# Kernel tuning notes

Hardware: AMD Instinct MI355X
Metric: run time of the kernel (lower is better)

Reference implementation:

```python
import jax, jax.numpy as jnp
import numpy as np

NUM_HEADS = 16


def setup_inputs() -> dict:
    key = jax.random.key(0)
    ks = jax.random.split(key, 4)
    B, S, H = 2, 2048, 1024
    hidden_states = jax.random.normal(ks[0], (B, S, H), dtype=jnp.float32)
    attention_mask = jnp.zeros((B, 1, 1, S), dtype=jnp.float32)
    scale = 1.0 / np.sqrt(H)
    Wq = jax.random.normal(ks[1], (H, H), dtype=jnp.float32) * scale
    Wk = jax.random.normal(ks[2], (H, H), dtype=jnp.float32) * scale
    Wv = jax.random.normal(ks[3], (H, H), dtype=jnp.float32) * scale
    bq = jnp.zeros((H,), dtype=jnp.float32)
    bk = jnp.zeros((H,), dtype=jnp.float32)
    bv = jnp.zeros((H,), dtype=jnp.float32)
    return {"hidden_states": hidden_states, "attention_mask": attention_mask,
            "Wq": Wq, "bq": bq, "Wk": Wk, "bk": bk, "Wv": Wv, "bv": bv}


def _split_heads(x, B, S):
    # [B, S, H] -> [B, h, S, d]
    return x.reshape(B, S, NUM_HEADS, -1).transpose(0, 2, 1, 3)


def reference(hidden_states, attention_mask, Wq, bq, Wk, bk, Wv, bv):
    B, S, H = hidden_states.shape
    d = H // NUM_HEADS
    q = _split_heads(hidden_states @ Wq + bq, B, S)  # [B,h,S,d]
    k = _split_heads(hidden_states @ Wk + bk, B, S)
    v = _split_heads(hidden_states @ Wv + bv, B, S)

    scores = jnp.einsum('bhqd,bhkd->bhqk', q, k) / jnp.sqrt(jnp.float32(d))
    # causal mask: -inf strictly above diagonal, plus additive pad mask
    i = jnp.arange(S)[:, None]
    j = jnp.arange(S)[None, :]
    causal = jnp.where(j > i, -jnp.inf, 0.0).astype(scores.dtype)  # [S,S]
    scores = scores + attention_mask + causal[None, None, :, :]

    probs = jax.nn.softmax(scores, axis=-1)  # dropout prob = 0.0 -> identity
    context = jnp.einsum('bhqk,bhkd->bhqd', probs, v)  # [B,h,S,d]
    return context.transpose(0, 2, 1, 3).reshape(B, S, H)
```

## Files before the change

### kernel.cpp

```cpp
#include <hip/hip_runtime.h>

typedef __attribute__((ext_vector_type(4)))  float f32x4;
typedef __attribute__((ext_vector_type(16))) float f32x16;
typedef __attribute__((ext_vector_type(8)))  short bf16x8;

typedef __attribute__((address_space(1))) const void gvoid;
typedef __attribute__((address_space(3))) void lvoid;

__device__ __forceinline__ void gl_lds16(const void* g, void* l) {
  __builtin_amdgcn_global_load_lds((gvoid*)g, (lvoid*)l, 16, 0, 0);
}

__device__ __forceinline__ float exp2_fast(float x) {
  return __builtin_amdgcn_exp2f(x);
}

__device__ __forceinline__ ushort f2bf(float f) {
  union { float f; unsigned u; } v; v.f = f;
  unsigned u = v.u;
  return (ushort)((u + 0x7fffu + ((u >> 16) & 1u)) >> 16);
}

__device__ __forceinline__ uint cvt_pk_bf16(float lo, float hi) {
  uint r;
  asm("v_cvt_pk_bf16_f32 %0, %1, %2" : "=v"(r) : "v"(lo), "v"(hi));
  return r;
}
__device__ __forceinline__ void plswap(uint& x, uint& y) {
  asm volatile("v_permlane32_swap_b32 %0, %1" : "+v"(x), "+v"(y));
}

__global__ __launch_bounds__(256) void cvt_x(const float* __restrict__ x,
                                             ushort* __restrict__ o) {
  int idx = blockIdx.x * 256 + threadIdx.x;
  float4 v = reinterpret_cast<const float4*>(x)[idx];
  ushort4 r;
  r.x = f2bf(v.x); r.y = f2bf(v.y); r.z = f2bf(v.z); r.w = f2bf(v.w);
  reinterpret_cast<ushort4*>(o)[idx] = r;
}

__global__ __launch_bounds__(256) void wtrans(const float* __restrict__ Wq,
                                              const float* __restrict__ Wk,
                                              const float* __restrict__ Wv,
                                              ushort* __restrict__ WT) {
  __shared__ ushort tile[64 * 68];
  int bx = blockIdx.x;
  int w = bx >> 8, rem = bx & 255;
  int k0 = (rem >> 4) << 6, n0 = (rem & 15) << 6;
  const float* W = (w == 0) ? Wq : (w == 1) ? Wk : Wv;
  int tid = threadIdx.x;
#pragma unroll
  for (int it = 0; it < 4; ++it) {
    int idx = tid + it * 256;
    int r = idx >> 4, c4 = (idx & 15) * 4;
    float4 v = *reinterpret_cast<const float4*>(&W[(k0 + r) * 1024 + n0 + c4]);
    ushort4 u;
    u.x = f2bf(v.x); u.y = f2bf(v.y); u.z = f2bf(v.z); u.w = f2bf(v.w);
    *reinterpret_cast<ushort4*>(&tile[r * 68 + c4]) = u;
  }
  __syncthreads();
#pragma unroll
  for (int it = 0; it < 4; ++it) {
    int idx = tid + it * 256;
    int n = idx >> 4, k4 = (idx & 15) * 4;
    ushort4 o;
    o.x = tile[(k4 + 0) * 68 + n];
    o.y = tile[(k4 + 1) * 68 + n];
    o.z = tile[(k4 + 2) * 68 + n];
    o.w = tile[(k4 + 3) * 68 + n];
    *reinterpret_cast<ushort4*>(&WT[w * 1048576 + (size_t)(n0 + n) * 1024 + k0 + k4]) = o;
  }
}

__global__ __launch_bounds__(256) void qkv_gemm(
    const ushort* __restrict__ Xb, const ushort* __restrict__ WT,
    const float* __restrict__ bq, const float* __restrict__ bk,
    const float* __restrict__ bv, ushort* __restrict__ Qb,
    ushort* __restrict__ Kb, ushort* __restrict__ VT) {
  __shared__ ushort smem[128 * 136];
  ushort* Xs = smem;
  ushort* Ws = smem + 8192;
  int tid = threadIdx.x;
  int wave = tid >> 6, lane = tid & 63, g = lane >> 4, lr = lane & 15;
  int wr = wave >> 1, wc = wave & 1;
  int m0 = blockIdx.x << 7;
  int n0g = blockIdx.y << 7;
  f32x4 acc[4][4];
#pragma unroll
  for (int i = 0; i < 4; ++i)
#pragma unroll
    for (int j = 0; j < 4; ++j) { acc[i][j][0] = 0.f; acc[i][j][1] = 0.f; acc[i][j][2] = 0.f; acc[i][j][3] = 0.f; }

  int l3 = lane >> 3;
  int jsw = ((lane & 7) ^ l3) * 8;
  int swz = lr & 7;
  for (int k0 = 0; k0 < 1024; k0 += 64) {
    __syncthreads();
#pragma unroll
    for (int c = 0; c < 4; ++c) {
      int cw = wave * 4 + c;
      int row = cw * 8 + l3;
      gl_lds16(Xb + (size_t)(m0 + row) * 1024 + k0 + jsw, Xs + cw * 512);
      gl_lds16(WT + (size_t)(n0g + row) * 1024 + k0 + jsw, Ws + cw * 512);
    }
    __syncthreads();
#pragma unroll
    for (int ks = 0; ks < 2; ++ks) {
      bf16x8 a[4], b[4];
      int slot = ((ks * 4 + g) ^ swz) * 8;
#pragma unroll
      for (int mi = 0; mi < 4; ++mi)
        a[mi] = *reinterpret_cast<const bf16x8*>(&Xs[(wr * 64 + mi * 16 + lr) * 64 + slot]);
#pragma unroll
      for (int ni = 0; ni < 4; ++ni)
        b[ni] = *reinterpret_cast<const bf16x8*>(&Ws[(wc * 64 + ni * 16 + lr) * 64 + slot]);
#pragma unroll
      for (int mi = 0; mi < 4; ++mi)
#pragma unroll
        for (int ni = 0; ni < 4; ++ni)
          acc[mi][ni] = __builtin_amdgcn_mfma_f32_16x16x32_bf16(a[mi], b[ni], acc[mi][ni], 0, 0, 0);
    }
  }
  __syncthreads();

  int which = n0g >> 10;
  const float* bias = (which == 0) ? bq : (which == 1) ? bk : bv;
  int nloc0 = (n0g & 1023);
  if (which == 2) {
#pragma unroll
    for (int ni = 0; ni < 4; ++ni) {
      int row = wc * 64 + ni * 16 + lr;
      float bb = bias[nloc0 + row];
#pragma unroll
      for (int mi = 0; mi < 4; ++mi) {
        int m = wr * 64 + mi * 16 + g * 4;
        ushort4 v4;
        v4.x = f2bf(acc[mi][ni][0] + bb);
        v4.y = f2bf(acc[mi][ni][1] + bb);
        v4.z = f2bf(acc[mi][ni][2] + bb);
        v4.w = f2bf(acc[mi][ni][3] + bb);
        *reinterpret_cast<ushort4*>(&smem[row * 136 + m]) = v4;
      }
    }
    __syncthreads();
    int b_ = m0 >> 11, s0 = m0 & 2047;
#pragma unroll
    for (int it = 0; it < 8; ++it) {
      int c = tid + it * 256;
      int row = c >> 4, mc = (c & 15) * 8;
      uint4 vv = *reinterpret_cast<const uint4*>(&smem[row * 136 + mc]);
      int n = nloc0 + row;
      int hh = n >> 6, dd = n & 63;
      *reinterpret_cast<uint4*>(&VT[((size_t)(b_ * 16 + hh) * 64 + dd) * 2048 + s0 + mc]) = vv;
    }
  } else {
#pragma unroll
    for (int ni = 0; ni < 4; ++ni) {
      int n = wc * 64 + ni * 16 + lr;
      float bb = bias[nloc0 + n];
#pragma unroll
      for (int mi = 0; mi < 4; ++mi) {
#pragma unroll
        for (int r = 0; r < 4; ++r)
          smem[(wr * 64 + mi * 16 + g * 4 + r) * 136 + n] = f2bf(acc[mi][ni][r] + bb);
      }
    }
    __syncthreads();
    ushort* ob = (which == 0) ? Qb : Kb;
#pragma unroll
    for (int it = 0; it < 8; ++it) {
      int c = tid + it * 256;
      int row = c >> 4, nc = (c & 15) * 8;
      uint4 vv = *reinterpret_cast<const uint4*>(&smem[row * 136 + nc]);
      int m = m0 + row;
      int b_ = m >> 11, s = m & 2047;
      int n = nloc0 + nc;
      int hh = n >> 6, dd = n & 63;
      *reinterpret_cast<uint4*>(&ob[((size_t)(b_ * 16 + hh) * 2048 + s) * 64 + dd]) = vv;
    }
  }
}

__device__ __forceinline__ void softmax_state(f32x16& s, float& mrun, float& lrun,
                                              f32x16& Od0, f32x16& Od1,
                                              bf16x8& p0, bf16x8& p1) {
  float tmx = s[0];
#pragma unroll
  for (int j = 1; j < 16; ++j) tmx = fmaxf(tmx, s[j]);
  tmx = fmaxf(tmx, __shfl_xor(tmx, 32));
  if (!__all(tmx - mrun <= 11.5f)) {
    float nm = fmaxf(mrun, tmx);
    float al = exp2_fast(mrun - nm);
    mrun = nm;
    lrun *= al;
#pragma unroll
    for (int j = 0; j < 16; ++j) { Od0[j] *= al; Od1[j] *= al; }
  }
  float rs = 0.f;
#pragma unroll
  for (int j = 0; j < 16; ++j) { float p = exp2_fast(s[j] - mrun); s[j] = p; rs += p; }
  rs += __shfl_xor(rs, 32);
  lrun += rs;
  uint x0 = cvt_pk_bf16(s[0], s[1]),   y0 = cvt_pk_bf16(s[4], s[5]);
  uint x1 = cvt_pk_bf16(s[2], s[3]),   y1 = cvt_pk_bf16(s[6], s[7]);
  plswap(x0, y0); plswap(x1, y1);
  uint x2 = cvt_pk_bf16(s[8], s[9]),   y2 = cvt_pk_bf16(s[12], s[13]);
  uint x3 = cvt_pk_bf16(s[10], s[11]), y3 = cvt_pk_bf16(s[14], s[15]);
  plswap(x2, y2); plswap(x3, y3);
  union U { uint w[4]; bf16x8 v; } u0, u1;
  u0.w[0] = x0; u0.w[1] = x1; u0.w[2] = y0; u0.w[3] = y1;
  u1.w[0] = x2; u1.w[1] = x3; u1.w[2] = y2; u1.w[3] = y3;
  p0 = u0.v; p1 = u1.v;
}

__device__ __forceinline__ void attn_stage2(const ushort* Kh, const ushort* VTh,
                                            char* smem, int buf, int kv0,
                                            int ws, int l3, int jsw) {
  ushort* Ksb = (ushort*)(smem + buf * 16384);
  ushort* Vsb = Ksb + 4096;
#pragma unroll
  for (int c = 0; c < 4; ++c) {
    int ch = ws * 4 + c;
    int row = ch * 8 + l3;
    gl_lds16(Kh + (size_t)(kv0 + row) * 64 + jsw, Ksb + ch * 512);
    gl_lds16(VTh + (size_t)row * 2048 + kv0 + jsw, Vsb + ch * 512);
  }
}

__device__ __forceinline__ void attn_writeout(char* smem, int wave, int lane,
                                              const f32x16& Od0, const f32x16& Od1,
                                              float lrun, float* outp, int q0w) {
  float* Ot = (float*)smem + wave * 2176;
  int hi = lane >> 5, l31 = lane & 31;
  float rl = 1.0f / lrun;
#pragma unroll
  for (int jj = 0; jj < 4; ++jj) {
    int d0a = jj * 8 + 4 * hi;
    float4 w0, w1;
    w0.x = Od0[jj * 4 + 0] * rl; w0.y = Od0[jj * 4 + 1] * rl;
    w0.z = Od0[jj * 4 + 2] * rl; w0.w = Od0[jj * 4 + 3] * rl;
    w1.x = Od1[jj * 4 + 0] * rl; w1.y = Od1[jj * 4 + 1] * rl;
    w1.z = Od1[jj * 4 + 2] * rl; w1.w = Od1[jj * 4 + 3] * rl;
    *reinterpret_cast<float4*>(&Ot[l31 * 68 + d0a]) = w0;
    *reinterpret_cast<float4*>(&Ot[l31 * 68 + 32 + d0a]) = w1;
  }
  int qr = lane >> 1, half = lane & 1;
  const float* Orow = &Ot[qr * 68 + half * 32];
  float* og = outp + (size_t)(q0w + qr) * 1024 + half * 32;
#pragma unroll
  for (int c2 = 0; c2 < 8; ++c2)
    *reinterpret_cast<float4*>(og + c2 * 4) = *reinterpret_cast<const float4*>(Orow + c2 * 4);
}

__global__ __launch_bounds__(256) void attn(const ushort* __restrict__ Qb,
                                            const ushort* __restrict__ Kb,
                                            const ushort* __restrict__ VT,
                                            const float* __restrict__ mask,
                                            float* __restrict__ out) {
  __shared__ char smem[65536];
  const float SCALE = 0.125f * 1.44269504f;
  const float L2E = 1.44269504f;
  int tid = threadIdx.x;
  int wave = tid >> 6, lane = tid & 63;
  int strip = wave & 1, P = wave >> 1;
  int hi = lane >> 5, l31 = lane & 31;
  int l3 = lane >> 3;
  int jsw = ((lane & 7) ^ l3) * 8;
  int bid = blockIdx.x;
  int logical = (bid & 7) * 64 + (bid >> 3);
  int pi = logical & 15, bh = logical >> 4;
  int b_ = bh >> 4, h = bh & 15;
  const ushort* Qh = Qb + (size_t)bh * 131072;
  const ushort* Kh = Kb + (size_t)bh * 131072;
  const ushort* VTh = VT + (size_t)bh * 131072;
  const float* maskp = mask + b_ * 2048;
  int qa0 = pi * 64 + strip * 32;
  int qb0 = (31 - pi) * 64 + strip * 32;
  int tmax = 31 - pi;
  int nsup = (tmax + 2) >> 1;

  bf16x8 aqa[4], aqb[4];
#pragma unroll
  for (int ds = 0; ds < 4; ++ds) {
    aqa[ds] = *reinterpret_cast<const bf16x8*>(Qh + (qa0 + l31) * 64 + ds * 16 + hi * 8);
    aqb[ds] = *reinterpret_cast<const bf16x8*>(Qh + (qb0 + l31) * 64 + ds * 16 + hi * 8);
  }

  f32x16 OA0, OA1, OB0, OB1;
#pragma unroll
  for (int j = 0; j < 16; ++j) { OA0[j] = 0.f; OA1[j] = 0.f; OB0[j] = 0.f; OB1[j] = 0.f; }
  float mA = -__builtin_inff(), lA = 0.f, mB = -__builtin_inff(), lB = 0.f;

  attn_stage2(Kh, VTh, smem, P, P << 6, strip, l3, jsw);

  for (int s = 0; s < nsup; ++s) {
    __syncthreads();
    int tn = 2 * (s + 1) + P;
    if (tn <= tmax)
      attn_stage2(Kh, VTh, smem, ((s + 1) & 1) * 2 + P, tn << 6, strip, l3, jsw);
    int t = 2 * s + P;
    if (t <= tmax) {
      ushort* Ksb = (ushort*)(smem + ((s & 1) * 2 + P) * 16384);
      ushort* Vsb = Ksb + 4096;
      int kv0 = t << 6;
#pragma unroll
      for (int sub = 0; sub < 2; ++sub) {
        int kvb = kv0 + sub * 32;
        bool actA = (kvb <= qa0), actB = (kvb <= qb0);
        if (!actB && !actA) continue;
        bf16x8 kf[4];
        int krow = sub * 32 + l31;
        int ksw = krow & 7;
#pragma unroll
        for (int ds = 0; ds < 4; ++ds)
          kf[ds] = *reinterpret_cast<const bf16x8*>(Ksb + krow * 64 + (((ds * 2 + hi) ^ ksw) * 8));
        f32x16 sB, sA;
        __builtin_amdgcn_s_setprio(1);
        if (actB) {
#pragma unroll
          for (int j = 0; j < 16; ++j) sB[j] = 0.f;
#pragma unroll
          for (int ds = 0; ds < 4; ++ds)
            sB = __builtin_amdgcn_mfma_f32_32x32x16_bf16(kf[ds], aqb[ds], sB, 0, 0, 0);
        }
        if (actA) {
#pragma unroll
          for (int j = 0; j < 16; ++j) sA[j] = 0.f;
#pragma unroll
          for (int ds = 0; ds < 4; ++ds)
            sA = __builtin_amdgcn_mfma_f32_32x32x16_bf16(kf[ds], aqa[ds], sA, 0, 0, 0);
        }
        __builtin_amdgcn_s_setprio(0);

        float4 mv[4];
#pragma unroll
        for (int jj = 0; jj < 4; ++jj) {
          mv[jj] = *reinterpret_cast<const float4*>(maskp + kvb + jj * 8 + 4 * hi);
          mv[jj].x *= L2E; mv[jj].y *= L2E; mv[jj].z *= L2E; mv[jj].w *= L2E;
        }

        bf16x8 pB0, pB1, pA0, pA1;
        if (actB) {
          bool dg = (kvb == qb0);
#pragma unroll
          for (int jj = 0; jj < 4; ++jj) {
            const float* mvp = (const float*)&mv[jj];
#pragma unroll
            for (int r = 0; r < 4; ++r) {
              int j = jj * 4 + r;
              float v = sB[j] * SCALE + mvp[r];
              if (dg) {
                int kvg = kvb + jj * 8 + 4 * hi + r;
                v = (kvg > qb0 + l31) ? -__builtin_inff() : v;
              }
              sB[j] = v;
            }
          }
          softmax_state(sB, mB, lB, OB0, OB1, pB0, pB1);
        }
        if (actA) {
          bool dg = (kvb == qa0);
#pragma unroll
          for (int jj = 0; jj < 4; ++jj) {
            const float* mvp = (const float*)&mv[jj];
#pragma unroll
            for (int r = 0; r < 4; ++r) {
              int j = jj * 4 + r;
              float v = sA[j] * SCALE + mvp[r];
              if (dg) {
                int kvg = kvb + jj * 8 + 4 * hi + r;
                v = (kvg > qa0 + l31) ? -__builtin_inff() : v;
              }
              sA[j] = v;
            }
          }
          softmax_state(sA, mA, lA, OA0, OA1, pA0, pA1);
        }

        __builtin_amdgcn_s_setprio(1);
#pragma unroll
        for (int ks = 0; ks < 2; ++ks) {
#pragma unroll
          for (int h2 = 0; h2 < 2; ++h2) {
            int drow = h2 * 32 + l31;
            bf16x8 vf = *reinterpret_cast<const bf16x8*>(
                Vsb + drow * 64 + (((sub * 4 + ks * 2 + hi) ^ (drow & 7)) * 8));
            if (actB) {
              f32x16& O = h2 ? OB1 : OB0;
              O = __builtin_amdgcn_mfma_f32_32x32x16_bf16(vf, ks ? pB1 : pB0, O, 0, 0, 0);
            }
            if (actA) {
              f32x16& O = h2 ? OA1 : OA0;
              O = __builtin_amdgcn_mfma_f32_32x32x16_bf16(vf, ks ? pA1 : pA0, O, 0, 0, 0);
            }
          }
        }
        __builtin_amdgcn_s_setprio(0);
      }
    }
  }

  __syncthreads();
  float* mb = (float*)smem;
  const int RS = 69;
  if (P == 1) {
    float* reg = mb + strip * (64 * RS) + lane * RS;
#pragma unroll
    for (int j = 0; j < 16; ++j) {
      reg[j]      = OA0[j];
      reg[16 + j] = OA1[j];
      reg[32 + j] = OB0[j];
      reg[48 + j] = OB1[j];
    }
    reg[64] = mA; reg[65] = lA; reg[66] = mB; reg[67] = lB;
  }
  __syncthreads();
  if (P == 0) {
    const float* reg = mb + strip * (64 * RS) + lane * RS;
    {
      float m2 = reg[64], l2 = reg[65];
      float nm = fmaxf(mA, m2);
      float a1 = exp2_fast(mA - nm), a2 = exp2_fast(m2 - nm);
#pragma unroll
      for (int j = 0; j < 16; ++j) {
        OA0[j] = OA0[j] * a1 + reg[j] * a2;
        OA1[j] = OA1[j] * a1 + reg[16 + j] * a2;
      }
      lA = lA * a1 + l2 * a2; mA = nm;
    }
    {
      float m2 = reg[66], l2 = reg[67];
      float nm = fmaxf(mB, m2);
      float a1 = exp2_fast(mB - nm), a2 = exp2_fast(m2 - nm);
#pragma unroll
      for (int j = 0; j < 16; ++j) {
        OB0[j] = OB0[j] * a1 + reg[32 + j] * a2;
        OB1[j] = OB1[j] * a1 + reg[48 + j] * a2;
      }
      lB = lB * a1 + l2 * a2; mB = nm;
    }
  }
  __syncthreads();
  if (P == 0) {
    float* outp = out + (size_t)b_ * 2048 * 1024 + h * 64;
    attn_writeout(smem, wave, lane, OA0, OA1, lA, outp, qa0);
    attn_writeout(smem, wave, lane, OB0, OB1, lB, outp, qb0);
  }
}

extern "C" void kernel_launch(void* const* d_in, const int* in_sizes, int n_in,
                              void* d_out, int out_size, void* d_ws, size_t ws_size,
                              hipStream_t stream) {
  const float* X    = (const float*)d_in[0];
  const float* mask = (const float*)d_in[1];
  const float* Wq   = (const float*)d_in[2];
  const float* bq   = (const float*)d_in[3];
  const float* Wk   = (const float*)d_in[4];
  const float* bk   = (const float*)d_in[5];
  const float* Wv   = (const float*)d_in[6];
  const float* bv   = (const float*)d_in[7];
  float* out = (float*)d_out;

  char* ws = (char*)d_ws;
  ushort* Xb  = (ushort*)ws;
  ushort* WTb = (ushort*)(ws + 8388608);
  ushort* Qb  = (ushort*)(ws + 8388608 + 6291456);
  ushort* Kb  = Qb + 4194304;
  ushort* VT  = Kb + 4194304;

  cvt_x<<<4096, 256, 0, stream>>>(X, Xb);
  wtrans<<<768, 256, 0, stream>>>(Wq, Wk, Wv, WTb);
  qkv_gemm<<<dim3(32, 24), 256, 0, stream>>>(Xb, WTb, bq, bk, bv, Qb, Kb, VT);
  attn<<<512, 256, 0, stream>>>(Qb, Kb, VT, mask, out);
}
```

Before: 229.9 us.

## Load K and V tiles directly from global memory instead of LDS staging

Removes the double-buffered global-to-LDS staging of K and V tiles and the per-iteration block barrier. Each wave now reads its K and V^T fragments straight from global memory into registers, relying on L2/L1 caching. Shared memory shrinks to about 35 KB, used only for the merge and writeout, which may raise occupancy. In exchange, loads are no longer shared across waves, cache traffic rises, and global-load latency now sits directly on each wave's critical path.

```diff
diff --git a/kernel.cpp b/kernel.cpp
--- a/kernel.cpp
+++ b/kernel.cpp
@@ -213,24 +213,10 @@
   p0 = u0.v; p1 = u1.v;
 }
 
-__device__ __forceinline__ void attn_stage2(const ushort* Kh, const ushort* VTh,
-                                            char* smem, int buf, int kv0,
-                                            int ws, int l3, int jsw) {
-  ushort* Ksb = (ushort*)(smem + buf * 16384);
-  ushort* Vsb = Ksb + 4096;
-#pragma unroll
-  for (int c = 0; c < 4; ++c) {
-    int ch = ws * 4 + c;
-    int row = ch * 8 + l3;
-    gl_lds16(Kh + (size_t)(kv0 + row) * 64 + jsw, Ksb + ch * 512);
-    gl_lds16(VTh + (size_t)row * 2048 + kv0 + jsw, Vsb + ch * 512);
-  }
-}
-
-__device__ __forceinline__ void attn_writeout(char* smem, int wave, int lane,
+__device__ __forceinline__ void attn_writeout(float* smf, int wave, int lane,
                                               const f32x16& Od0, const f32x16& Od1,
                                               float lrun, float* outp, int q0w) {
-  float* Ot = (float*)smem + wave * 2176;
+  float* Ot = smf + wave * 2176;
   int hi = lane >> 5, l31 = lane & 31;
   float rl = 1.0f / lrun;
 #pragma unroll
@@ -257,15 +243,13 @@
                                             const ushort* __restrict__ VT,
                                             const float* __restrict__ mask,
                                             float* __restrict__ out) {
-  __shared__ char smem[65536];
+  __shared__ float smf[8832];
   const float SCALE = 0.125f * 1.44269504f;
   const float L2E = 1.44269504f;
   int tid = threadIdx.x;
   int wave = tid >> 6, lane = tid & 63;
   int strip = wave & 1, P = wave >> 1;
   int hi = lane >> 5, l31 = lane & 31;
-  int l3 = lane >> 3;
-  int jsw = ((lane & 7) ^ l3) * 8;
   int bid = blockIdx.x;
   int logical = (bid & 7) * 64 + (bid >> 3);
   int pi = logical & 15, bh = logical >> 4;
@@ -277,7 +261,6 @@
   int qa0 = pi * 64 + strip * 32;
   int qb0 = (31 - pi) * 64 + strip * 32;
   int tmax = 31 - pi;
-  int nsup = (tmax + 2) >> 1;
 
   bf16x8 aqa[4], aqb[4];
 #pragma unroll
@@ -291,120 +274,117 @@
   for (int j = 0; j < 16; ++j) { OA0[j] = 0.f; OA1[j] = 0.f; OB0[j] = 0.f; OB1[j] = 0.f; }
   float mA = -__builtin_inff(), lA = 0.f, mB = -__builtin_inff(), lB = 0.f;
 
-  attn_stage2(Kh, VTh, smem, P, P << 6, strip, l3, jsw);
-
-  for (int s = 0; s < nsup; ++s) {
-    __syncthreads();
-    int tn = 2 * (s + 1) + P;
-    if (tn <= tmax)
-      attn_stage2(Kh, VTh, smem, ((s + 1) & 1) * 2 + P, tn << 6, strip, l3, jsw);
-    int t = 2 * s + P;
-    if (t <= tmax) {
-      ushort* Ksb = (ushort*)(smem + ((s & 1) * 2 + P) * 16384);
-      ushort* Vsb = Ksb + 4096;
-      int kv0 = t << 6;
-#pragma unroll
-      for (int sub = 0; sub < 2; ++sub) {
-        int kvb = kv0 + sub * 32;
-        bool actA = (kvb <= qa0), actB = (kvb <= qb0);
-        if (!actB && !actA) continue;
-        bf16x8 kf[4];
-        int krow = sub * 32 + l31;
-        int ksw = krow & 7;
+  for (int t = P; t <= tmax; t += 2) {
+    int kv0 = t << 6;
+#pragma unroll
+    for (int sub = 0; sub < 2; ++sub) {
+      int kvb = kv0 + sub * 32;
+      bool actA = (kvb <= qa0), actB = (kvb <= qb0);
+      if (!actB && !actA) continue;
+
+      const ushort* Kt = Kh + (size_t)kvb * 64 + l31 * 64 + hi * 8;
+      bf16x8 kf[4];
+#pragma unroll
+      for (int ds = 0; ds < 4; ++ds)
+        kf[ds] = *reinterpret_cast<const bf16x8*>(Kt + ds * 16);
+
+      f32x16 sB, sA;
+      __builtin_amdgcn_s_setprio(1);
+      if (actB) {
+#pragma unroll
+        for (int j = 0; j < 16; ++j) sB[j] = 0.f;
 #pragma unroll
         for (int ds = 0; ds < 4; ++ds)
-          kf[ds] = *reinterpret_cast<const bf16x8*>(Ksb + krow * 64 + (((ds * 2 + hi) ^ ksw) * 8));
-        f32x16 sB, sA;
-        __builtin_amdgcn_s_setprio(1);
-        if (actB) {
-#pragma unroll
-          for (int j = 0; j < 16; ++j) sB[j] = 0.f;
-#pragma unroll
-          for (int ds = 0; ds < 4; ++ds)
-            sB = __builtin_amdgcn_mfma_f32_32x32x16_bf16(kf[ds], aqb[ds], sB, 0, 0, 0);
+          sB = __builtin_amdgcn_mfma_f32_32x32x16_bf16(kf[ds], aqb[ds], sB, 0, 0, 0);
+      }
+      if (actA) {
+#pragma unroll
+        for (int j = 0; j < 16; ++j) sA[j] = 0.f;
+#pragma unroll
+        for (int ds = 0; ds < 4; ++ds)
+          sA = __builtin_amdgcn_mfma_f32_32x32x16_bf16(kf[ds], aqa[ds], sA, 0, 0, 0);
+      }
+      __builtin_amdgcn_s_setprio(0);
+
+      bf16x8 vf[4];
+#pragma unroll
+      for (int ks = 0; ks < 2; ++ks)
+#pragma unroll
+        for (int h2 = 0; h2 < 2; ++h2) {
+          int drow = h2 * 32 + l31;
+          vf[ks * 2 + h2] = *reinterpret_cast<const bf16x8*>(
+              VTh + (size_t)drow * 2048 + kvb + ks * 16 + hi * 8);
         }
-        if (actA) {
-#pragma unroll
-          for (int j = 0; j < 16; ++j) sA[j] = 0.f;
-#pragma unroll
-          for (int ds = 0; ds < 4; ++ds)
-            sA = __builtin_amdgcn_mfma_f32_32x32x16_bf16(kf[ds], aqa[ds], sA, 0, 0, 0);
-        }
-        __builtin_amdgcn_s_setprio(0);
-
-        float4 mv[4];
+
+      float4 mv[4];
+#pragma unroll
+      for (int jj = 0; jj < 4; ++jj) {
+        mv[jj] = *reinterpret_cast<const float4*>(maskp + kvb + jj * 8 + 4 * hi);
+        mv[jj].x *= L2E; mv[jj].y *= L2E; mv[jj].z *= L2E; mv[jj].w *= L2E;
+      }
+
+      bf16x8 pB0, pB1, pA0, pA1;
+      if (actB) {
+        bool dg = (kvb == qb0);
 #pragma unroll
         for (int jj = 0; jj < 4; ++jj) {
-          mv[jj] = *reinterpret_cast<const float4*>(maskp + kvb + jj * 8 + 4 * hi);
-          mv[jj].x *= L2E; mv[jj].y *= L2E; mv[jj].z *= L2E; mv[jj].w *= L2E;
-        }
-
-        bf16x8 pB0, pB1, pA0, pA1;
-        if (actB) {
-          bool dg = (kvb == qb0);
-#pragma unroll
-          for (int jj = 0; jj < 4; ++jj) {
-            const float* mvp = (const float*)&mv[jj];
-#pragma unroll
-            for (int r = 0; r < 4; ++r) {
-              int j = jj * 4 + r;
-              float v = sB[j] * SCALE + mvp[r];
-              if (dg) {
-                int kvg = kvb + jj * 8 + 4 * hi + r;
-                v = (kvg > qb0 + l31) ? -__builtin_inff() : v;
-              }
-              sB[j] = v;
+          const float* mvp = (const float*)&mv[jj];
+#pragma unroll
+          for (int r = 0; r < 4; ++r) {
+            int j = jj * 4 + r;
+            float v = sB[j] * SCALE + mvp[r];
+            if (dg) {
+              int kvg = kvb + jj * 8 + 4 * hi + r;
+              v = (kvg > qb0 + l31) ? -__builtin_inff() : v;
             }
-          }
-          softmax_state(sB, mB, lB, OB0, OB1, pB0, pB1);
-        }
-        if (actA) {
-          bool dg = (kvb == qa0);
-#pragma unroll
-          for (int jj = 0; jj < 4; ++jj) {
-            const float* mvp = (const float*)&mv[jj];
-#pragma unroll
-            for (int r = 0; r < 4; ++r) {
-              int j = jj * 4 + r;
-              float v = sA[j] * SCALE + mvp[r];
-              if (dg) {
-                int kvg = kvb + jj * 8 + 4 * hi + r;
-                v = (kvg > qa0 + l31) ? -__builtin_inff() : v;
-              }
-              sA[j] = v;
-            }
-          }
-          softmax_state(sA, mA, lA, OA0, OA1, pA0, pA1);
-        }
-
-        __builtin_amdgcn_s_setprio(1);
-#pragma unroll
-        for (int ks = 0; ks < 2; ++ks) {
-#pragma unroll
-          for (int h2 = 0; h2 < 2; ++h2) {
-            int drow = h2 * 32 + l31;
-            bf16x8 vf = *reinterpret_cast<const bf16x8*>(
-                Vsb + drow * 64 + (((sub * 4 + ks * 2 + hi) ^ (drow & 7)) * 8));
-            if (actB) {
-              f32x16& O = h2 ? OB1 : OB0;
-              O = __builtin_amdgcn_mfma_f32_32x32x16_bf16(vf, ks ? pB1 : pB0, O, 0, 0, 0);
-            }
-            if (actA) {
-              f32x16& O = h2 ? OA1 : OA0;
-              O = __builtin_amdgcn_mfma_f32_32x32x16_bf16(vf, ks ? pA1 : pA0, O, 0, 0, 0);
-            }
+            sB[j] = v;
           }
         }
-        __builtin_amdgcn_s_setprio(0);
-      }
+        softmax_state(sB, mB, lB, OB0, OB1, pB0, pB1);
+      }
+      if (actA) {
+        bool dg = (kvb == qa0);
+#pragma unroll
+        for (int jj = 0; jj < 4; ++jj) {
+          const float* mvp = (const float*)&mv[jj];
+#pragma unroll
+          for (int r = 0; r < 4; ++r) {
+            int j = jj * 4 + r;
+            float v = sA[j] * SCALE + mvp[r];
+            if (dg) {
+              int kvg = kvb + jj * 8 + 4 * hi + r;
+              v = (kvg > qa0 + l31) ? -__builtin_inff() : v;
+            }
+            sA[j] = v;
+          }
+        }
+        softmax_state(sA, mA, lA, OA0, OA1, pA0, pA1);
+      }
+
+      __builtin_amdgcn_s_setprio(1);
+#pragma unroll
+      for (int ks = 0; ks < 2; ++ks) {
+#pragma unroll
+        for (int h2 = 0; h2 < 2; ++h2) {
+          bf16x8 vv = vf[ks * 2 + h2];
+          if (actB) {
+            f32x16& O = h2 ? OB1 : OB0;
+            O = __builtin_amdgcn_mfma_f32_32x32x16_bf16(vv, ks ? pB1 : pB0, O, 0, 0, 0);
+          }
+          if (actA) {
+            f32x16& O = h2 ? OA1 : OA0;
+            O = __builtin_amdgcn_mfma_f32_32x32x16_bf16(vv, ks ? pA1 : pA0, O, 0, 0, 0);
+          }
+        }
+      }
+      __builtin_amdgcn_s_setprio(0);
     }
   }
 
   __syncthreads();
-  float* mb = (float*)smem;
   const int RS = 69;
   if (P == 1) {
-    float* reg = mb + strip * (64 * RS) + lane * RS;
+    float* reg = smf + strip * (64 * RS) + lane * RS;
 #pragma unroll
     for (int j = 0; j < 16; ++j) {
       reg[j]      = OA0[j];
@@ -416,7 +396,7 @@
   }
   __syncthreads();
   if (P == 0) {
-    const float* reg = mb + strip * (64 * RS) + lane * RS;
+    const float* reg = smf + strip * (64 * RS) + lane * RS;
     {
       float m2 = reg[64], l2 = reg[65];
       float nm = fmaxf(mA, m2);
@@ -443,8 +423,8 @@
   __syncthreads();
   if (P == 0) {
     float* outp = out + (size_t)b_ * 2048 * 1024 + h * 64;
-    attn_writeout(smem, wave, lane, OA0, OA1, lA, outp, qa0);
-    attn_writeout(smem, wave, lane, OB0, OB1, lB, outp, qb0);
+    attn_writeout(smf, wave, lane, OA0, OA1, lA, outp, qa0);
+    attn_writeout(smf, wave, lane, OB0, OB1, lB, outp, qb0);
   }
 }
 
```

After: 240.3 us. 4.5% more time.
